# Kernel optimization log

Hardware: AMD Instinct MI355X
Metric: run time of the kernel (lower is better)

## Reference

```python
import jax, jax.numpy as jnp
import numpy as np

B, N, R = 16, 512, 10
DE, DR, DOUT = 256, 64, 256

def setup_inputs() -> dict:
    key = jax.random.key(0)
    k1, k2, k3, k4 = jax.random.split(key, 4)
    node_features = jax.random.normal(k1, (B, N, DE), dtype=jnp.float32)
    relation_features = jax.random.normal(k2, (B, R, DR), dtype=jnp.float32)
    adj = jax.random.uniform(k3, (B, R, N, N), dtype=jnp.float32)
    in_dim = (DE + DR) * R
    bound = float(np.sqrt(6.0 / (in_dim + DOUT)))  # xavier_uniform
    W = jax.random.uniform(k4, (DOUT, in_dim), dtype=jnp.float32, minval=-bound, maxval=bound)
    bias = jnp.zeros((DOUT,), dtype=jnp.float32)
    return {"node_features": node_features, "relation_features": relation_features,
            "adj": adj, "W": W, "bias": bias}

def reference(node_features, relation_features, adj, W, bias):
    # adj: [B,R,N,N]; node_features: [B,N,De]; relation_features: [B,R,Dr]
    # Per relation r: bmm(adj[:,r], cat([node, rel_r broadcast], -1))
    # Node part: adj @ node_features for every relation at once.
    node_part = jnp.einsum('brnm,bmd->brnd', adj, node_features)      # [B,R,N,De]
    # Relation part: adj @ (rel_r repeated over rows) == rowsum(adj) * rel_r
    rel_part = adj.sum(axis=-1)[..., None] * relation_features[:, :, None, :]  # [B,R,N,Dr]
    supports = jnp.concatenate([node_part, rel_part], axis=-1)        # [B,R,N,De+Dr]
    supports = supports.transpose(0, 2, 1, 3).reshape(node_features.shape[0],
                                                      node_features.shape[1], -1)  # [B,N,R*(De+Dr)]
    return supports @ W.T + bias
```

## Files before the change

### kernel.cpp

```cpp
#include <hip/hip_runtime.h>
#include <stdint.h>

#define B_     16
#define N_     512
#define R_     10
#define DE_    256
#define DR_    64
#define DOUT_  256
#define INDIM_ 3200
#define BLK_   320
#define RN_    5120
#define SPLITS_ 4
#define CPS_    20

typedef __bf16          v8bf  __attribute__((ext_vector_type(8)));
typedef unsigned short  v8us  __attribute__((ext_vector_type(8)));
typedef unsigned short  v4us  __attribute__((ext_vector_type(4)));
typedef float           f32x4 __attribute__((ext_vector_type(4)));

static __device__ __forceinline__ unsigned short f2b(float f) {
  union { float f; unsigned u; } c; c.f = f;
  unsigned r = c.u + 0x7FFFu + ((c.u >> 16) & 1u);
  return (unsigned short)(r >> 16);
}

static __device__ __forceinline__ v8bf us2bf(v8us u) {
  union { v8us u; v8bf b; } c; c.u = u; return c.b;
}

static __device__ __forceinline__ void gl_lds16(const void* g, void* l) {
  __builtin_amdgcn_global_load_lds(
      (const __attribute__((address_space(1))) void*)g,
      (__attribute__((address_space(3))) void*)l, 16, 0, 0);
}

static __device__ __forceinline__ void waitv12() { asm volatile("s_waitcnt vmcnt(12)" ::: "memory"); }
static __device__ __forceinline__ void waitv8()  { asm volatile("s_waitcnt vmcnt(8)"  ::: "memory"); }
static __device__ __forceinline__ void waitv0()  { asm volatile("s_waitcnt vmcnt(0)"  ::: "memory"); }
static __device__ __forceinline__ void waitl0()  { asm volatile("s_waitcnt lgkmcnt(0)" ::: "memory"); }
#define SCHED0() __builtin_amdgcn_sched_barrier(0)

__global__ void prep_all(const float* __restrict__ nf, const float* __restrict__ W,
                         const float* __restrict__ rel,
                         unsigned short* __restrict__ nodeB,
                         unsigned short* __restrict__ WnB,
                         float* __restrict__ Uf) {
  const int bb = blockIdx.x;
  const int tid = threadIdx.x;
  if (bb < 256) {
    const size_t base = (size_t)bb * 8192;
#pragma unroll
    for (int p = 0; p < 4; ++p) {
      size_t off = base + (size_t)p * 2048 + (size_t)tid * 8;
      float4 x = *(const float4*)(nf + off);
      float4 y = *(const float4*)(nf + off + 4);
      v8us u;
      u[0] = f2b(x.x); u[1] = f2b(x.y); u[2] = f2b(x.z); u[3] = f2b(x.w);
      u[4] = f2b(y.x); u[5] = f2b(y.y); u[6] = f2b(y.z); u[7] = f2b(y.w);
      *(v8us*)(nodeB + off) = u;
    }
  } else if (bb < 896) {
    int idx = (bb - 256) * 1024 + tid * 4;
    int r = idx >> 16;
    int o = (idx >> 8) & 255;
    int d = idx & 255;
    float4 x = *(const float4*)(W + (size_t)o * INDIM_ + r * BLK_ + d);
    v4us u;
    u[0] = f2b(x.x); u[1] = f2b(x.y); u[2] = f2b(x.z); u[3] = f2b(x.w);
    *(v4us*)(WnB + idx) = u;
  } else {
    int idx = (bb - 896) * 256 + tid;
    int o  = idx & 255;
    int br = idx >> 8;
    int r  = br % R_;
    const float* rp = rel + (size_t)br * DR_;
    const float* wp = W + (size_t)o * INDIM_ + r * BLK_ + DE_;
    float v = 0.f;
#pragma unroll 8
    for (int d = 0; d < DR_; ++d) v += rp[d] * wp[d];
    Uf[idx] = v;
  }
}

__global__ void stageA_gemm(const unsigned short* __restrict__ nodeB,
                            const unsigned short* __restrict__ WnB,
                            const float* __restrict__ Uf,
                            unsigned short* __restrict__ Gp) {
  __shared__ unsigned short S[2 * 16384];
  const int br = blockIdx.x;
  const int b  = br / R_, r = br % R_;
  const int o0 = blockIdx.y * 128;
  const int m0 = blockIdx.z * 128;
  const int tid  = threadIdx.x;
  const int lane = tid & 63;
  const int wave = tid >> 6;
  const int wm = wave >> 1, wn = wave & 1;
  const int quad = lane >> 4, l16 = lane & 15;

  const unsigned short* Wb = WnB + (size_t)r * (DOUT_ * DE_);
  const unsigned short* Nb = nodeB + (size_t)b * (N_ * DE_);

  f32x4 acc[4][4];
#pragma unroll
  for (int i = 0; i < 4; ++i)
#pragma unroll
    for (int j = 0; j < 4; ++j) acc[i][j] = f32x4{0.f, 0.f, 0.f, 0.f};

  const int srl = lane >> 3;
  const int skc = lane & 7;

  {
    unsigned short* Al = S;
    unsigned short* Bl = S + 8192;
#pragma unroll
    for (int it = 0; it < 4; ++it) {
      int rowblk = it * 32 + wave * 8;
      int rl = rowblk + srl;
      int kc = skc ^ (rl & 7);
      gl_lds16(Wb + (size_t)(o0 + rl) * DE_ + kc * 8, Al + rowblk * 64);
      gl_lds16(Nb + (size_t)(m0 + rl) * DE_ + kc * 8, Bl + rowblk * 64);
    }
  }
  __syncthreads();

  for (int t = 0; t < 4; ++t) {
    unsigned short* Sc = S + (t & 1) * 16384;
    unsigned short* Sn = S + ((t & 1) ^ 1) * 16384;
    if (t < 3) {
      const int dk = (t + 1) * 64;
      unsigned short* Aln = Sn;
      unsigned short* Bln = Sn + 8192;
#pragma unroll
      for (int it = 0; it < 4; ++it) {
        int rowblk = it * 32 + wave * 8;
        int rl = rowblk + srl;
        int kc = skc ^ (rl & 7);
        gl_lds16(Wb + (size_t)(o0 + rl) * DE_ + dk + kc * 8, Aln + rowblk * 64);
        gl_lds16(Nb + (size_t)(m0 + rl) * DE_ + dk + kc * 8, Bln + rowblk * 64);
      }
    }
    const unsigned short* Al = Sc;
    const unsigned short* Bl = Sc + 8192;
#pragma unroll
    for (int ks = 0; ks < 2; ++ks) {
      const int kb = ks * 4;
      v8bf av[4], bv[4];
#pragma unroll
      for (int mi = 0; mi < 4; ++mi) {
        int m = wm * 64 + mi * 16 + l16;
        av[mi] = us2bf(*(const v8us*)(Al + m * 64 + (((kb + quad) ^ (m & 7)) * 8)));
      }
#pragma unroll
      for (int ni = 0; ni < 4; ++ni) {
        int c = wn * 64 + ni * 16 + l16;
        bv[ni] = us2bf(*(const v8us*)(Bl + c * 64 + (((kb + quad) ^ (c & 7)) * 8)));
      }
#pragma unroll
      for (int mi = 0; mi < 4; ++mi)
#pragma unroll
        for (int ni = 0; ni < 4; ++ni)
          acc[mi][ni] = __builtin_amdgcn_mfma_f32_16x16x32_bf16(av[mi], bv[ni], acc[mi][ni], 0, 0, 0);
    }
    __syncthreads();
  }

#pragma unroll
  for (int mi = 0; mi < 4; ++mi)
#pragma unroll
    for (int t = 0; t < 4; ++t) {
      int o_loc = wm * 64 + mi * 16 + quad * 4 + t;
      float u = Uf[(size_t)br * DOUT_ + o0 + o_loc];
#pragma unroll
      for (int ni = 0; ni < 4; ++ni) {
        int m_loc = wn * 64 + ni * 16 + l16;
        S[o_loc * 128 + m_loc] = f2b(acc[mi][ni][t] + u);
      }
    }
  __syncthreads();
#pragma unroll
  for (int p = 0; p < 8; ++p) {
    int idx16 = p * 2048 + tid * 8;
    int orow = idx16 >> 7;
    int moff = idx16 & 127;
    unsigned short* dst = Gp + ((size_t)(b * DOUT_ + o0 + orow)) * RN_ + r * N_ + m0 + moff;
    *(v8us*)dst = *(const v8us*)(S + idx16);
  }
}

__global__ __launch_bounds__(512, 1)
void stageB_gemm(const float* __restrict__ adj,
                 const unsigned short* __restrict__ Gp,
                 float* __restrict__ part) {
  __shared__ unsigned short SB[65536];
  unsigned short* Bring = SB;
  unsigned short* Aring = SB + 49152;
  const int b  = blockIdx.x;
  const int n0 = blockIdx.y * 128;
  const int sp = blockIdx.z;
  const int tid  = threadIdx.x;
  const int lane = tid & 63;
  const int wave = tid >> 6;
  const int wm = wave >> 2;
  const int wn = wave & 3;
  const int quad = lane >> 4, l16 = lane & 15;

  const float* Ab = adj + (size_t)b * (R_ * N_ * N_);
  const unsigned short* Gb = Gp + (size_t)b * (DOUT_ * RN_);

  f32x4 acc[4][4];
#pragma unroll
  for (int i = 0; i < 4; ++i)
#pragma unroll
    for (int j = 0; j < 4; ++j) acc[i][j] = f32x4{0.f, 0.f, 0.f, 0.f};

  const int ar0 = tid >> 3;
  const int ac8 = tid & 7;
  const int acs = ac8 ^ (ar0 & 7);
  const int brl = wave * 8 + (lane >> 3);
  const int bkc = lane & 7;
  const int c0 = sp * CPS_;

  float4 As[3][4];

#define ISSUE_B(slot, cc) do { \
    unsigned short* Bd = Bring + (slot) * 16384; \
    const int k0b = (cc) << 6; \
    _Pragma("unroll") \
    for (int s = 0; s < 4; ++s) { \
      int rl = s * 64 + brl; \
      int kc = bkc ^ (rl & 7); \
      gl_lds16(Gb + (size_t)rl * RN_ + k0b + kc * 8, Bd + (s * 64 + wave * 8) * 64); \
    } } while (0)

#define ISSUE_A(set, cc) do { \
    const float* g = Ab + ((size_t)((cc) >> 3) * N_ + n0) * N_ + ((cc) & 7) * 64 \
                     + (size_t)ar0 * N_ + ac8 * 8; \
    As[set][0] = *(const float4*)(g); \
    As[set][1] = *(const float4*)(g + 4); \
    As[set][2] = *(const float4*)(g + 64 * N_); \
    As[set][3] = *(const float4*)(g + 64 * N_ + 4); } while (0)

#define CONV_A(set, abuf) do { \
    v8us u0, u1; \
    u0[0] = f2b(As[set][0].x); u0[1] = f2b(As[set][0].y); \
    u0[2] = f2b(As[set][0].z); u0[3] = f2b(As[set][0].w); \
    u0[4] = f2b(As[set][1].x); u0[5] = f2b(As[set][1].y); \
    u0[6] = f2b(As[set][1].z); u0[7] = f2b(As[set][1].w); \
    u1[0] = f2b(As[set][2].x); u1[1] = f2b(As[set][2].y); \
    u1[2] = f2b(As[set][2].z); u1[3] = f2b(As[set][2].w); \
    u1[4] = f2b(As[set][3].x); u1[5] = f2b(As[set][3].y); \
    u1[6] = f2b(As[set][3].z); u1[7] = f2b(As[set][3].w); \
    unsigned short* Ad = Aring + (abuf) * 8192; \
    *(v8us*)(Ad + ar0 * 64 + acs * 8) = u0; \
    *(v8us*)(Ad + (ar0 + 64) * 64 + acs * 8) = u1; } while (0)

#define COMPUTE(bslot, abuf) do { \
    const unsigned short* Alc = Aring + (abuf) * 8192; \
    const unsigned short* Blc = Bring + (bslot) * 16384; \
    _Pragma("unroll") \
    for (int ks = 0; ks < 2; ++ks) { \
      const int kb = ks * 4; \
      v8bf av[4], bv[4]; \
      _Pragma("unroll") \
      for (int mi = 0; mi < 4; ++mi) { \
        int m = wm * 64 + mi * 16 + l16; \
        av[mi] = us2bf(*(const v8us*)(Alc + m * 64 + (((kb + quad) ^ (m & 7)) * 8))); \
      } \
      _Pragma("unroll") \
      for (int ni = 0; ni < 4; ++ni) { \
        int o = wn * 64 + ni * 16 + l16; \
        bv[ni] = us2bf(*(const v8us*)(Blc + o * 64 + (((kb + quad) ^ (o & 7)) * 8))); \
      } \
      _Pragma("unroll") \
      for (int mi = 0; mi < 4; ++mi) \
        _Pragma("unroll") \
        for (int ni = 0; ni < 4; ++ni) \
          acc[mi][ni] = __builtin_amdgcn_mfma_f32_16x16x32_bf16(av[mi], bv[ni], acc[mi][ni], 0, 0, 0); \
    } } while (0)

  ISSUE_B(0, c0 + 0); SCHED0();
  ISSUE_A(0, c0 + 0); SCHED0();
  ISSUE_B(1, c0 + 1); SCHED0();
  ISSUE_A(1, c0 + 1); SCHED0();
  ISSUE_A(2, c0 + 2); SCHED0();
  waitv12();
  SCHED0();
  CONV_A(0, 0);
  waitl0();

#pragma unroll
  for (int t = 0; t < CPS_; ++t) {
    __builtin_amdgcn_s_barrier();
    SCHED0();
    if (t + 2 < CPS_) { ISSUE_B((t + 2) % 3, c0 + t + 2); }
    SCHED0();
    if (t + 3 < CPS_) { ISSUE_A((t + 3) % 3, c0 + t + 3); }
    SCHED0();
    COMPUTE(t % 3, t & 1);
    if (t + 1 < CPS_) {
      if (t < 17)       waitv12();
      else if (t == 17) waitv8();
      else              waitv0();
      SCHED0();
      CONV_A((t + 1) % 3, (t + 1) & 1);
    }
    waitl0();
  }

#undef ISSUE_B
#undef ISSUE_A
#undef CONV_A
#undef COMPUTE

  float* pb = part + (((size_t)sp * B_ + b) * N_) * DOUT_;
#pragma unroll
  for (int mi = 0; mi < 4; ++mi)
#pragma unroll
    for (int t4 = 0; t4 < 4; ++t4) {
      int row = n0 + wm * 64 + mi * 16 + quad * 4 + t4;
#pragma unroll
      for (int ni = 0; ni < 4; ++ni) {
        int col = wn * 64 + ni * 16 + l16;
        pb[(size_t)row * DOUT_ + col] = acc[mi][ni][t4];
      }
    }
}

__global__ void reduce_out(const float* __restrict__ part, const float* __restrict__ bias,
                           float* __restrict__ out) {
  const size_t idx = (size_t)blockIdx.x * 256 + threadIdx.x;
  const size_t stride = (size_t)B_ * N_ * DOUT_ / 4;
  f32x4 a = *(const f32x4*)(bias + (idx & 63) * 4);
#pragma unroll
  for (int s = 0; s < SPLITS_; ++s) {
    f32x4 p = *(const f32x4*)((const float*)part + (stride * s + idx) * 4);
    a += p;
  }
  *(f32x4*)(out + idx * 4) = a;
}

extern "C" void kernel_launch(void* const* d_in, const int* in_sizes, int n_in,
                              void* d_out, int out_size, void* d_ws, size_t ws_size,
                              hipStream_t stream) {
  const float* node = (const float*)d_in[0];
  const float* rel  = (const float*)d_in[1];
  const float* adj  = (const float*)d_in[2];
  const float* W    = (const float*)d_in[3];
  const float* bias = (const float*)d_in[4];
  float* out = (float*)d_out;

  char* ws = (char*)d_ws;
  unsigned short* nodeB = (unsigned short*)(ws);
  unsigned short* WnB   = (unsigned short*)(ws + ((size_t)5 << 20));
  float*          Uf    = (float*)         (ws + ((size_t)7 << 20));
  unsigned short* Gp    = (unsigned short*)(ws + ((size_t)8 << 20));
  float*          part  = (float*)         (ws + ((size_t)48 << 20));

  prep_all<<<dim3(1056), 256, 0, stream>>>(node, W, rel, nodeB, WnB, Uf);
  stageA_gemm<<<dim3(B_ * R_, DOUT_ / 128, N_ / 128), 256, 0, stream>>>(nodeB, WnB, Uf, Gp);
  stageB_gemm<<<dim3(B_, N_ / 128, SPLITS_), 512, 0, stream>>>(adj, Gp, part);
  reduce_out<<<dim3((B_ * N_ * DOUT_ / 4) / 256), 256, 0, stream>>>(part, bias, out);
}
```

Baseline: 300.5 us.

## Replace triple-buffered stageB ring with two-slot ping-pong and single-buffer stageA

In stageB, the three-slot LDS ring (B tiles prefetched two chunks ahead, A registers three ahead) is replaced by a two-slot ping-pong. Each slot holds both the A and B tiles, and vmcnt waits are simplified. This cuts LDS use and register pressure from the A staging registers. StageA drops its double buffering and loads each K-chunk into a single buffer followed by a barrier. Both changes shorten prefetch depth, so global latency is hidden less well; stageA also risks a missing barrier before its buffer is overwritten.

```diff
diff --git a/kernel.cpp b/kernel.cpp
--- a/kernel.cpp
+++ b/kernel.cpp
@@ -34,10 +34,9 @@
       (__attribute__((address_space(3))) void*)l, 16, 0, 0);
 }
 
-static __device__ __forceinline__ void waitv12() { asm volatile("s_waitcnt vmcnt(12)" ::: "memory"); }
-static __device__ __forceinline__ void waitv8()  { asm volatile("s_waitcnt vmcnt(8)"  ::: "memory"); }
-static __device__ __forceinline__ void waitv0()  { asm volatile("s_waitcnt vmcnt(0)"  ::: "memory"); }
-static __device__ __forceinline__ void waitl0()  { asm volatile("s_waitcnt lgkmcnt(0)" ::: "memory"); }
+static __device__ __forceinline__ void waitv4() { asm volatile("s_waitcnt vmcnt(4)" ::: "memory"); }
+static __device__ __forceinline__ void waitv0() { asm volatile("s_waitcnt vmcnt(0)" ::: "memory"); }
+static __device__ __forceinline__ void waitl0() { asm volatile("s_waitcnt lgkmcnt(0)" ::: "memory"); }
 #define SCHED0() __builtin_amdgcn_sched_barrier(0)
 
 __global__ void prep_all(const float* __restrict__ nf, const float* __restrict__ W,
@@ -86,7 +85,9 @@
                             const unsigned short* __restrict__ WnB,
                             const float* __restrict__ Uf,
                             unsigned short* __restrict__ Gp) {
-  __shared__ unsigned short S[2 * 16384];
+  __shared__ unsigned short S[128 * 128];
+  unsigned short* Al = S;
+  unsigned short* Bl = S + 128 * 64;
   const int br = blockIdx.x;
   const int b  = br / R_, r = br % R_;
   const int o0 = blockIdx.y * 128;
@@ -106,41 +107,16 @@
 #pragma unroll
     for (int j = 0; j < 4; ++j) acc[i][j] = f32x4{0.f, 0.f, 0.f, 0.f};
 
-  const int srl = lane >> 3;
-  const int skc = lane & 7;
-
-  {
-    unsigned short* Al = S;
-    unsigned short* Bl = S + 8192;
+  for (int dk = 0; dk < DE_; dk += 64) {
 #pragma unroll
     for (int it = 0; it < 4; ++it) {
       int rowblk = it * 32 + wave * 8;
-      int rl = rowblk + srl;
-      int kc = skc ^ (rl & 7);
-      gl_lds16(Wb + (size_t)(o0 + rl) * DE_ + kc * 8, Al + rowblk * 64);
-      gl_lds16(Nb + (size_t)(m0 + rl) * DE_ + kc * 8, Bl + rowblk * 64);
-    }
-  }
-  __syncthreads();
-
-  for (int t = 0; t < 4; ++t) {
-    unsigned short* Sc = S + (t & 1) * 16384;
-    unsigned short* Sn = S + ((t & 1) ^ 1) * 16384;
-    if (t < 3) {
-      const int dk = (t + 1) * 64;
-      unsigned short* Aln = Sn;
-      unsigned short* Bln = Sn + 8192;
-#pragma unroll
-      for (int it = 0; it < 4; ++it) {
-        int rowblk = it * 32 + wave * 8;
-        int rl = rowblk + srl;
-        int kc = skc ^ (rl & 7);
-        gl_lds16(Wb + (size_t)(o0 + rl) * DE_ + dk + kc * 8, Aln + rowblk * 64);
-        gl_lds16(Nb + (size_t)(m0 + rl) * DE_ + dk + kc * 8, Bln + rowblk * 64);
-      }
-    }
-    const unsigned short* Al = Sc;
-    const unsigned short* Bl = Sc + 8192;
+      int rl = rowblk + (lane >> 3);
+      int kc = (lane & 7) ^ (rl & 7);
+      gl_lds16(Wb + (size_t)(o0 + rl) * DE_ + dk + kc * 8, Al + rowblk * 64);
+      gl_lds16(Nb + (size_t)(m0 + rl) * DE_ + dk + kc * 8, Bl + rowblk * 64);
+    }
+    __syncthreads();
 #pragma unroll
     for (int ks = 0; ks < 2; ++ks) {
       const int kb = ks * 4;
@@ -191,9 +167,7 @@
 void stageB_gemm(const float* __restrict__ adj,
                  const unsigned short* __restrict__ Gp,
                  float* __restrict__ part) {
-  __shared__ unsigned short SB[65536];
-  unsigned short* Bring = SB;
-  unsigned short* Aring = SB + 49152;
+  __shared__ unsigned short SB[2 * 24576];
   const int b  = blockIdx.x;
   const int n0 = blockIdx.y * 128;
   const int sp = blockIdx.z;
@@ -220,10 +194,10 @@
   const int bkc = lane & 7;
   const int c0 = sp * CPS_;
 
-  float4 As[3][4];
+  float4 As0[4], As1[4];
 
 #define ISSUE_B(slot, cc) do { \
-    unsigned short* Bd = Bring + (slot) * 16384; \
+    unsigned short* Bd = SB + (slot) * 24576 + 8192; \
     const int k0b = (cc) << 6; \
     _Pragma("unroll") \
     for (int s = 0; s < 4; ++s) { \
@@ -232,31 +206,27 @@
       gl_lds16(Gb + (size_t)rl * RN_ + k0b + kc * 8, Bd + (s * 64 + wave * 8) * 64); \
     } } while (0)
 
-#define ISSUE_A(set, cc) do { \
+#define ISSUE_A(AR, cc) do { \
     const float* g = Ab + ((size_t)((cc) >> 3) * N_ + n0) * N_ + ((cc) & 7) * 64 \
                      + (size_t)ar0 * N_ + ac8 * 8; \
-    As[set][0] = *(const float4*)(g); \
-    As[set][1] = *(const float4*)(g + 4); \
-    As[set][2] = *(const float4*)(g + 64 * N_); \
-    As[set][3] = *(const float4*)(g + 64 * N_ + 4); } while (0)
-
-#define CONV_A(set, abuf) do { \
+    AR[0] = *(const float4*)(g); \
+    AR[1] = *(const float4*)(g + 4); \
+    AR[2] = *(const float4*)(g + 64 * N_); \
+    AR[3] = *(const float4*)(g + 64 * N_ + 4); } while (0)
+
+#define CONV_A(AR, slot) do { \
     v8us u0, u1; \
-    u0[0] = f2b(As[set][0].x); u0[1] = f2b(As[set][0].y); \
-    u0[2] = f2b(As[set][0].z); u0[3] = f2b(As[set][0].w); \
-    u0[4] = f2b(As[set][1].x); u0[5] = f2b(As[set][1].y); \
-    u0[6] = f2b(As[set][1].z); u0[7] = f2b(As[set][1].w); \
-    u1[0] = f2b(As[set][2].x); u1[1] = f2b(As[set][2].y); \
-    u1[2] = f2b(As[set][2].z); u1[3] = f2b(As[set][2].w); \
-    u1[4] = f2b(As[set][3].x); u1[5] = f2b(As[set][3].y); \
-    u1[6] = f2b(As[set][3].z); u1[7] = f2b(As[set][3].w); \
-    unsigned short* Ad = Aring + (abuf) * 8192; \
+    u0[0] = f2b(AR[0].x); u0[1] = f2b(AR[0].y); u0[2] = f2b(AR[0].z); u0[3] = f2b(AR[0].w); \
+    u0[4] = f2b(AR[1].x); u0[5] = f2b(AR[1].y); u0[6] = f2b(AR[1].z); u0[7] = f2b(AR[1].w); \
+    u1[0] = f2b(AR[2].x); u1[1] = f2b(AR[2].y); u1[2] = f2b(AR[2].z); u1[3] = f2b(AR[2].w); \
+    u1[4] = f2b(AR[3].x); u1[5] = f2b(AR[3].y); u1[6] = f2b(AR[3].z); u1[7] = f2b(AR[3].w); \
+    unsigned short* Ad = SB + (slot) * 24576; \
     *(v8us*)(Ad + ar0 * 64 + acs * 8) = u0; \
     *(v8us*)(Ad + (ar0 + 64) * 64 + acs * 8) = u1; } while (0)
 
-#define COMPUTE(bslot, abuf) do { \
-    const unsigned short* Alc = Aring + (abuf) * 8192; \
-    const unsigned short* Blc = Bring + (bslot) * 16384; \
+#define COMPUTE(slot) do { \
+    const unsigned short* Alc = SB + (slot) * 24576; \
+    const unsigned short* Blc = Alc + 8192; \
     _Pragma("unroll") \
     for (int ks = 0; ks < 2; ++ks) { \
       const int kb = ks * 4; \
@@ -278,33 +248,45 @@
           acc[mi][ni] = __builtin_amdgcn_mfma_f32_16x16x32_bf16(av[mi], bv[ni], acc[mi][ni], 0, 0, 0); \
     } } while (0)
 
-  ISSUE_B(0, c0 + 0); SCHED0();
-  ISSUE_A(0, c0 + 0); SCHED0();
-  ISSUE_B(1, c0 + 1); SCHED0();
-  ISSUE_A(1, c0 + 1); SCHED0();
-  ISSUE_A(2, c0 + 2); SCHED0();
-  waitv12();
+  ISSUE_A(As0, c0 + 0);
+  ISSUE_B(0, c0 + 0);
+  ISSUE_A(As1, c0 + 1);
+  waitv4();
   SCHED0();
-  CONV_A(0, 0);
+  CONV_A(As0, 0);
   waitl0();
-
-#pragma unroll
-  for (int t = 0; t < CPS_; ++t) {
-    __builtin_amdgcn_s_barrier();
-    SCHED0();
-    if (t + 2 < CPS_) { ISSUE_B((t + 2) % 3, c0 + t + 2); }
-    SCHED0();
-    if (t + 3 < CPS_) { ISSUE_A((t + 3) % 3, c0 + t + 3); }
-    SCHED0();
-    COMPUTE(t % 3, t & 1);
-    if (t + 1 < CPS_) {
-      if (t < 17)       waitv12();
-      else if (t == 17) waitv8();
+  __builtin_amdgcn_s_barrier();
+
+  for (int t = 0; t < CPS_; t += 2) {
+    {
+      ISSUE_B(1, c0 + t + 1);
+      if (t + 2 < CPS_) ISSUE_A(As0, c0 + t + 2);
+      SCHED0();
+      COMPUTE(0);
+      if (t + 2 < CPS_) waitv4();
       else              waitv0();
       SCHED0();
-      CONV_A((t + 1) % 3, (t + 1) & 1);
-    }
-    waitl0();
+      CONV_A(As1, 1);
+      waitl0();
+      __builtin_amdgcn_s_barrier();
+    }
+    {
+      if (t + 2 < CPS_) {
+        ISSUE_B(0, c0 + t + 2);
+        if (t + 3 < CPS_) ISSUE_A(As1, c0 + t + 3);
+        SCHED0();
+        COMPUTE(1);
+        if (t + 3 < CPS_) waitv4();
+        else              waitv0();
+        SCHED0();
+        CONV_A(As0, 0);
+        waitl0();
+        __builtin_amdgcn_s_barrier();
+      } else {
+        SCHED0();
+        COMPUTE(1);
+      }
+    }
   }
 
 #undef ISSUE_B
```

Result: faster. 291.2 us (-3.1%).
